# Kernel tuning notes

Hardware: AMD Instinct MI355X
Metric: run time of the kernel (lower is better)

The kernel has to match this reference:

```python
import jax, jax.numpy as jnp
import numpy as np

NEG = -1e6  # mask value used by d2l-style masked_softmax


def masked_softmax(scores, valid_lens):
    # scores: [B, Q, K]; valid_lens: [B] int — mask key positions j >= valid_len
    K = scores.shape[-1]
    mask = jnp.arange(K, dtype=jnp.int32)[None, None, :] < valid_lens[:, None, None]
    scores = jnp.where(mask, scores, NEG)
    return jax.nn.softmax(scores, axis=-1)


def setup_inputs() -> dict:
    key = jax.random.key(0)
    kq, kk, kv, kl = jax.random.split(key, 4)
    B, Q, K, d = 16, 4096, 4096, 128
    queries = jax.random.normal(kq, (B, Q, d), dtype=jnp.float32)
    keys = jax.random.normal(kk, (B, K, d), dtype=jnp.float32)
    values = jax.random.normal(kv, (B, K, d), dtype=jnp.float32)
    valid_lens = jax.random.randint(kl, (B,), 1, K + 1, dtype=jnp.int32)
    return {"queries": queries, "keys": keys, "values": values,
            "valid_lens": valid_lens}


def reference(queries, keys, values, valid_lens):
    d = queries.shape[-1]
    # [B, Q, K] scores = Q K^T / sqrt(d)
    scores = jnp.einsum('bqd,bkd->bqk', queries, keys) / jnp.sqrt(
        jnp.asarray(d, queries.dtype))
    attn = masked_softmax(scores, valid_lens)
    # dropout is identity in eval mode
    return jnp.einsum('bqk,bkd->bqd', attn, values)
```

## Files before the change

kernel.cpp:

```cpp
#include <hip/hip_runtime.h>
#include <stdint.h>

typedef __attribute__((ext_vector_type(8))) short short8;
typedef __attribute__((ext_vector_type(4))) float float4v;
typedef __attribute__((ext_vector_type(16))) float f32x16;

#define B_  16
#define S_  4096
#define D_  128
#define TM  64
#define TN  64
#define NT_ (S_ / TN)
#define IMG 8192

#define ZERO16 {0.f,0.f,0.f,0.f, 0.f,0.f,0.f,0.f, 0.f,0.f,0.f,0.f, 0.f,0.f,0.f,0.f}

__device__ __forceinline__ unsigned short f2bf(float f) {
    union { float f; uint32_t u; } c; c.f = f;
    uint32_t u = c.u + 0x7FFFu + ((c.u >> 16) & 1u);
    return (unsigned short)(u >> 16);
}

__device__ __forceinline__ uint4 pack8(float4v x, float4v y) {
    uint4 r;
    r.x = (uint32_t)f2bf(x[0]) | ((uint32_t)f2bf(x[1]) << 16);
    r.y = (uint32_t)f2bf(x[2]) | ((uint32_t)f2bf(x[3]) << 16);
    r.z = (uint32_t)f2bf(y[0]) | ((uint32_t)f2bf(y[1]) << 16);
    r.w = (uint32_t)f2bf(y[2]) | ((uint32_t)f2bf(y[3]) << 16);
    return r;
}

__device__ __forceinline__ void gload16(const unsigned short* g, unsigned short* l) {
    __builtin_amdgcn_global_load_lds(
        (const __attribute__((address_space(1))) unsigned int*)g,
        (__attribute__((address_space(3))) unsigned int*)l, 16, 0, 0);
}

__device__ __forceinline__ uint32_t cvtpk(float lo, float hi) {
    uint32_t w;
    asm("v_cvt_pk_bf16_f32 %0, %1, %2" : "=v"(w) : "v"(lo), "v"(hi));
    return w;
}

__device__ __forceinline__ short8 build_pfrag(const float* p) {
    uint32_t xa = cvtpk(p[0], p[1]);
    uint32_t xb = cvtpk(p[2], p[3]);
    uint32_t ya = cvtpk(p[4], p[5]);
    uint32_t yb = cvtpk(p[6], p[7]);
    asm("v_permlane32_swap_b32 %0, %1" : "+v"(xa), "+v"(ya));
    asm("v_permlane32_swap_b32 %0, %1" : "+v"(xb), "+v"(yb));
    union { uint32_t u[4]; short8 s; } r;
    r.u[0] = xa; r.u[1] = xb; r.u[2] = ya; r.u[3] = yb;
    return r.s;
}

__global__ __launch_bounds__(256)
void prepass(const float* __restrict__ Kg, const float* __restrict__ Vg,
             unsigned short* __restrict__ Kb, unsigned short* __restrict__ Vb)
{
    const int t = threadIdx.x;
    const int tile = blockIdx.x, b = blockIdx.y;
    const size_t img = (size_t)(b * NT_ + tile) * IMG;

    const float* ksrc = Kg + ((size_t)b * S_ + tile * TN) * D_;
    const float* vsrc = Vg + ((size_t)b * S_ + tile * TN) * D_;
    unsigned short* kdst = Kb + img;
    unsigned short* vdst = Vb + img;

    float4v kx[4], ky[4];
    #pragma unroll
    for (int i = 0; i < 4; ++i) {
        int bid = i * 256 + t;
        int row = bid >> 4, cbp = bid & 15;
        int cb  = cbp ^ (row & 15);
        const float* s = ksrc + row * D_ + cb * 8;
        kx[i] = *(const float4v*)s;
        ky[i] = *(const float4v*)(s + 4);
    }
    const int kb = t >> 5, cg = t & 31;
    float4v v[8];
    #pragma unroll
    for (int r = 0; r < 8; ++r)
        v[r] = *(const float4v*)(vsrc + (kb * 8 + r) * D_ + cg * 4);

    #pragma unroll
    for (int i = 0; i < 4; ++i) {
        int bid = i * 256 + t;
        *(uint4*)(kdst + (size_t)bid * 8) = pack8(kx[i], ky[i]);
    }

    #pragma unroll
    for (int j = 0; j < 4; ++j) {
        int dr = cg * 4 + j;
        uint4 w;
        w.x = (uint32_t)f2bf(v[0][j]) | ((uint32_t)f2bf(v[1][j]) << 16);
        w.y = (uint32_t)f2bf(v[2][j]) | ((uint32_t)f2bf(v[3][j]) << 16);
        w.z = (uint32_t)f2bf(v[4][j]) | ((uint32_t)f2bf(v[5][j]) << 16);
        w.w = (uint32_t)f2bf(v[6][j]) | ((uint32_t)f2bf(v[7][j]) << 16);
        *(uint4*)(vdst + dr * 64 + (kb ^ (dr & 7)) * 8) = w;
    }
}

__global__ __launch_bounds__(256, 4)
void attn_fwd(const float* __restrict__ Qg,
              const unsigned short* __restrict__ Kb,
              const unsigned short* __restrict__ Vb,
              const int* __restrict__ VL,
              float* __restrict__ Og)
{
    __shared__ __align__(16) unsigned short SM[2 * IMG];
    __shared__ float Ls[128];
    unsigned short* Ks = SM;
    unsigned short* Vt = SM + IMG;

    const int t    = threadIdx.x;
    const int wave = t >> 6;
    const int lane = t & 63;
    const int l31  = lane & 31;
    const int hi   = lane >> 5;
    const int wq   = wave >> 1;
    const int wk   = wave & 1;

    const int b  = blockIdx.y;
    const int q0 = blockIdx.x * TM;
    const int nvalid = VL[b];
    const int ntiles = (nvalid + TN - 1) / TN;

    const float qscale = 0.08838834764831845f * 1.4426950408889634f;

    short8 qf[8];
    {
        const float* qp = Qg + ((size_t)b * S_ + (q0 + wq * 32 + l31)) * D_;
        #pragma unroll
        for (int ks = 0; ks < 8; ++ks) {
            float4v x = *(const float4v*)(qp + ks * 16 + hi * 8);
            float4v y = *(const float4v*)(qp + ks * 16 + hi * 8 + 4);
            #pragma unroll
            for (int j = 0; j < 4; ++j) { x[j] *= qscale; y[j] *= qscale; }
            union { uint4 u; short8 s; } cv; cv.u = pack8(x, y);
            qf[ks] = cv.s;
        }
    }

    f32x16 zz = ZERO16;
    f32x16 oacc[4];
    oacc[0] = zz; oacc[1] = zz; oacc[2] = zz; oacc[3] = zz;
    float lsum = 0.f;

    const int swk = l31 & 15;
    const int swv = l31 & 7;

    for (int tile = 0; tile < ntiles; ++tile) {
        const int n0 = tile * TN;
        __syncthreads();

        {
            const unsigned short* kimg = Kb + (size_t)(b * NT_ + tile) * IMG;
            const unsigned short* vimg = Vb + (size_t)(b * NT_ + tile) * IMG;
            #pragma unroll
            for (int i = 0; i < 4; ++i) {
                int go = (i * 256 + t) * 8;
                int lo = (i * 256 + wave * 64) * 8;
                gload16(kimg + go, &Ks[lo]);
                gload16(vimg + go, &Vt[lo]);
            }
        }
        __syncthreads();

        f32x16 st = zz;
        {
            const unsigned short* k0 = &Ks[(wk * 32 + l31) * D_];
            __builtin_amdgcn_s_setprio(1);
            #pragma unroll
            for (int ks = 0; ks < 8; ++ks) {
                int sl = (((ks << 1) | hi) ^ swk) << 3;
                short8 a0 = *(const short8*)(k0 + sl);
                st = __builtin_amdgcn_mfma_f32_32x32x16_bf16(a0, qf[ks], st, 0, 0, 0);
            }
            __builtin_amdgcn_s_setprio(0);
        }

        float p[16];
        const bool full = (n0 + TN) <= nvalid;
        if (full) {
            #pragma unroll
            for (int r = 0; r < 16; ++r) { p[r] = exp2f(st[r]); lsum += p[r]; }
        } else {
            #pragma unroll
            for (int r = 0; r < 16; ++r) {
                int key = n0 + wk * 32 + (r & 3) + 8 * (r >> 2) + 4 * hi;
                float e = exp2f(st[r]);
                p[r] = (key < nvalid) ? e : 0.f; lsum += p[r];
            }
        }

        short8 pf0 = build_pfrag(p);
        short8 pf1 = build_pfrag(p + 8);

        __builtin_amdgcn_s_setprio(1);
        #pragma unroll
        for (int dt = 0; dt < 4; ++dt) {
            const unsigned short* vrow = &Vt[(dt * 32 + l31) * TN];
            int s0 = ((((wk * 2 + 0) << 1) | hi) ^ swv) << 3;
            int s1 = ((((wk * 2 + 1) << 1) | hi) ^ swv) << 3;
            short8 v0 = *(const short8*)(vrow + s0);
            short8 v1 = *(const short8*)(vrow + s1);
            oacc[dt] = __builtin_amdgcn_mfma_f32_32x32x16_bf16(pf0, v0, oacc[dt], 0, 0, 0);
            oacc[dt] = __builtin_amdgcn_mfma_f32_32x32x16_bf16(pf1, v1, oacc[dt], 0, 0, 0);
        }
        __builtin_amdgcn_s_setprio(0);
    }

    float lpart = lsum + __shfl_xor(lsum, 32);

    float* red = (float*)SM;
    __syncthreads();
    if (wk == 1) {
        #pragma unroll
        for (int dt = 0; dt < 4; ++dt)
            #pragma unroll
            for (int r = 0; r < 16; ++r)
                red[(dt * 16 + r) * 128 + wq * 64 + lane] = oacc[dt][r];
        Ls[wq * 64 + lane] = lpart;
    }
    __syncthreads();
    if (wk == 0) {
        #pragma unroll
        for (int dt = 0; dt < 4; ++dt)
            #pragma unroll
            for (int r = 0; r < 16; ++r)
                oacc[dt][r] += red[(dt * 16 + r) * 128 + wq * 64 + lane];

        float ltot = lpart + Ls[wq * 64 + lane];
        float inv  = 1.0f / ltot;

        float* op = Og + ((size_t)b * S_ + (q0 + wq * 32)) * D_ + l31;
        #pragma unroll
        for (int r = 0; r < 16; ++r) {
            const int qc = (r & 3) + 8 * (r >> 2);
            float invr = __shfl(inv, qc + 4 * hi, 32);
            #pragma unroll
            for (int dt = 0; dt < 4; ++dt)
                op[(qc + 4 * hi) * D_ + dt * 32] = oacc[dt][r] * invr;
        }
    }
}

extern "C" void kernel_launch(void* const* d_in, const int* in_sizes, int n_in,
                              void* d_out, int out_size, void* d_ws, size_t ws_size,
                              hipStream_t stream) {
    const float* Q = (const float*)d_in[0];
    const float* K = (const float*)d_in[1];
    const float* V = (const float*)d_in[2];
    const int*   L = (const int*)d_in[3];
    float*       O = (float*)d_out;

    unsigned short* Kb = (unsigned short*)d_ws;
    unsigned short* Vb = Kb + (size_t)B_ * S_ * D_;

    dim3 grid(NT_, B_);
    prepass<<<grid, 256, 0, stream>>>(K, V, Kb, Vb);
    dim3 grid2(S_ / TM, B_);
    attn_fwd<<<grid2, 256, 0, stream>>>(Q, Kb, Vb, L, O);
}
```

Baseline: 275.1 us.

## Overlap next-tile K/V global loads with current-tile compute via staggered prefetch

Replaces the load-then-sync-then-compute loop with a software pipeline. After the QK^T MFMAs finish reading K, the next tile's K is issued into shared memory. After the PV MFMAs finish reading V, the next tile's V is issued. Partial vmcnt waits and raw s_barriers keep each buffer consistent, so global load latency hides behind the softmax and MFMA work. This depends on the hand-written waitcnt counts matching the number of gload16 ops. On the last tile it issues one redundant reload.

```diff
diff --git a/kernel.cpp b/kernel.cpp
--- a/kernel.cpp
+++ b/kernel.cpp
@@ -126,6 +126,9 @@
     const int nvalid = VL[b];
     const int ntiles = (nvalid + TN - 1) / TN;
 
+    const unsigned short* kbase = Kb + (size_t)b * NT_ * IMG;
+    const unsigned short* vbase = Vb + (size_t)b * NT_ * IMG;
+
     const float qscale = 0.08838834764831845f * 1.4426950408889634f;
 
     short8 qf[8];
@@ -150,22 +153,24 @@
     const int swk = l31 & 15;
     const int swv = l31 & 7;
 
+    {
+        const unsigned short* kimg = kbase;
+        #pragma unroll
+        for (int i = 0; i < 4; ++i)
+            gload16(kimg + (i * 256 + t) * 8, &Ks[(i * 256 + wave * 64) * 8]);
+        const unsigned short* vimg = vbase;
+        #pragma unroll
+        for (int i = 0; i < 4; ++i)
+            gload16(vimg + (i * 256 + t) * 8, &Vt[(i * 256 + wave * 64) * 8]);
+    }
+
     for (int tile = 0; tile < ntiles; ++tile) {
         const int n0 = tile * TN;
-        __syncthreads();
-
-        {
-            const unsigned short* kimg = Kb + (size_t)(b * NT_ + tile) * IMG;
-            const unsigned short* vimg = Vb + (size_t)(b * NT_ + tile) * IMG;
-            #pragma unroll
-            for (int i = 0; i < 4; ++i) {
-                int go = (i * 256 + t) * 8;
-                int lo = (i * 256 + wave * 64) * 8;
-                gload16(kimg + go, &Ks[lo]);
-                gload16(vimg + go, &Vt[lo]);
-            }
-        }
-        __syncthreads();
+        const int nx = (tile + 1 < ntiles) ? tile + 1 : tile;
+
+        asm volatile("s_waitcnt vmcnt(4)" ::: "memory");
+        __builtin_amdgcn_sched_barrier(0);
+        __builtin_amdgcn_s_barrier();
 
         f32x16 st = zz;
         {
@@ -180,6 +185,17 @@
             __builtin_amdgcn_s_setprio(0);
         }
 
+        asm volatile("s_waitcnt lgkmcnt(0)" ::: "memory");
+        __builtin_amdgcn_sched_barrier(0);
+        __builtin_amdgcn_s_barrier();
+
+        {
+            const unsigned short* kimg = kbase + (size_t)nx * IMG;
+            #pragma unroll
+            for (int i = 0; i < 4; ++i)
+                gload16(kimg + (i * 256 + t) * 8, &Ks[(i * 256 + wave * 64) * 8]);
+        }
+
         float p[16];
         const bool full = (n0 + TN) <= nvalid;
         if (full) {
@@ -193,9 +209,12 @@
                 p[r] = (key < nvalid) ? e : 0.f; lsum += p[r];
             }
         }
-
         short8 pf0 = build_pfrag(p);
         short8 pf1 = build_pfrag(p + 8);
+
+        asm volatile("s_waitcnt vmcnt(4)" ::: "memory");
+        __builtin_amdgcn_sched_barrier(0);
+        __builtin_amdgcn_s_barrier();
 
         __builtin_amdgcn_s_setprio(1);
         #pragma unroll
@@ -209,7 +228,21 @@
             oacc[dt] = __builtin_amdgcn_mfma_f32_32x32x16_bf16(pf1, v1, oacc[dt], 0, 0, 0);
         }
         __builtin_amdgcn_s_setprio(0);
-    }
+
+        asm volatile("s_waitcnt lgkmcnt(0)" ::: "memory");
+        __builtin_amdgcn_sched_barrier(0);
+        __builtin_amdgcn_s_barrier();
+
+        {
+            const unsigned short* vimg = vbase + (size_t)nx * IMG;
+            #pragma unroll
+            for (int i = 0; i < 4; ++i)
+                gload16(vimg + (i * 256 + t) * 8, &Vt[(i * 256 + wave * 64) * 8]);
+        }
+    }
+
+    asm volatile("s_waitcnt vmcnt(0)" ::: "memory");
+    __builtin_amdgcn_sched_barrier(0);
 
     float lpart = lsum + __shfl_xor(lsum, 32);
 
```

Result: slower. 550.8 us (+100.2%).
